# Kernel tuning notes

Hardware: AMD Instinct MI355X
Metric: run time of the kernel (lower is better)

## Reference

```python
import jax, jax.numpy as jnp
import numpy as np

D_MODEL = 2048
N_EXPERTS = 64
TOP_K = 2
AUX_LOSS_COEF = 0.01
ENTROPY_COEF = 0.01


def setup_inputs() -> dict:
    key = jax.random.key(0)
    kx, kw = jax.random.split(key)
    x = jax.random.normal(kx, (4, 4096, D_MODEL), dtype=jnp.float32)
    # nn.Linear(d_model, n_experts, bias=False) weight: [E, D]
    W = jax.random.normal(kw, (N_EXPERTS, D_MODEL), dtype=jnp.float32) * 0.02
    temp = jnp.ones((1,), dtype=jnp.float32)
    return {"x": x, "W": W, "temp": temp}


def reference(x, W, temp):
    B, S, D = x.shape
    E = W.shape[0]
    # gate logits: [B,S,E]
    logits = jnp.einsum("bsd,ed->bse", x, W)
    t = jnp.clip(temp, 0.1, 5.0)  # self.temp.clamp(0.1, 5.0); eval mode -> no noise
    probs = jax.nn.softmax(logits / t, axis=-1)
    expert_probs, expert_indices = jax.lax.top_k(probs, TOP_K)  # [B,S,K]
    # scatter ones at top-k indices -> [B,S,E]
    expert_mask = jax.nn.one_hot(expert_indices, E, dtype=probs.dtype).sum(axis=-2)
    # aux losses
    importance = probs.mean(axis=(0, 1))                 # [E]
    load = expert_mask.sum(axis=(0, 1)) / (B * S + 1e-6)  # [E]
    aux_load_loss = (importance * load).sum() * E * AUX_LOSS_COEF
    token_entropy = -(probs * jnp.log(jnp.clip(probs, 1e-8))).sum(axis=-1).mean()
    router_entropy = token_entropy * ENTROPY_COEF
    return (expert_probs, expert_indices, expert_mask, aux_load_loss, router_entropy)
```

## Files before the change

### kernel.cpp

```cpp
#include <hip/hip_runtime.h>
#include <hip/hip_bf16.h>
#include <math.h>

#define D_MODEL 2048
#define N_EXP   64
#define NTOK    16384
#define NBLK    512
#define NSTG    16

typedef short bf16x8 __attribute__((ext_vector_type(8)));
typedef float f32x16 __attribute__((ext_vector_type(16)));
typedef unsigned int u32;

#define OFF_PROBS 0
#define OFF_IDX   32768
#define OFF_MASK  65536
#define OFF_AUX   1114112
#define OFF_ENT   1114113

#define WF_PS 16384

#define MEMFENCE asm volatile("" ::: "memory")
#define FULLBAR() do { MEMFENCE; __builtin_amdgcn_s_barrier(); MEMFENCE; \
                       __builtin_amdgcn_sched_barrier(0); } while (0)

__device__ __forceinline__ void split3(float xv, u32& h, u32& m, u32& l) {
  u32 xb = __builtin_bit_cast(u32, xv);
  u32 hb = xb & 0xFFFF0000u;
  float tf = xv - __builtin_bit_cast(float, hb);
  u32 tb = __builtin_bit_cast(u32, tf);
  u32 mb = tb & 0xFFFF0000u;
  float t2 = tf - __builtin_bit_cast(float, mb);
  u32 lb = __builtin_bit_cast(u32, t2);
  h = hb >> 16; m = mb >> 16; l = lb >> 16;
}

__device__ __forceinline__ bool better(float a, int ia, float b, int ib) {
  return (a > b) || (a == b && ia < ib);
}

__global__ __launch_bounds__(256) void wprep_kernel(
    const float* __restrict__ W, bf16x8* __restrict__ Wf) {
  int gid  = blockIdx.x * 256 + threadIdx.x;
  int g    = gid >> 7;
  int n    = (gid >> 6) & 1;
  int lane = gid & 63;
  int e    = n * 32 + (lane & 31);
  int k    = g * 16 + ((lane >> 5) << 3);
  const float* wr = W + (size_t)e * D_MODEL + k;
  bf16x8 hv, mv, lv;
#pragma unroll
  for (int j = 0; j < 8; ++j) {
    u32 h, m, l;
    split3(wr[j], h, m, l);
    hv[j] = (short)h; mv[j] = (short)m; lv[j] = (short)l;
  }
  Wf[gid]             = hv;
  Wf[WF_PS + gid]     = mv;
  Wf[2 * WF_PS + gid] = lv;
}

__global__ __launch_bounds__(512, 4) void fused_kernel(
    const float* __restrict__ x, const bf16x8* __restrict__ Wf,
    const float* __restrict__ temp, float* __restrict__ out,
    float* __restrict__ imp_part, float* __restrict__ load_part,
    float* __restrict__ ent_part) {
  __shared__ float lds[16384];
  const int tid  = threadIdx.x;
  const int w    = tid >> 6;
  const int lane = tid & 63;
  const int t0   = blockIdx.x * 32;
  const int rl   = lane & 31;
  const int hg   = lane >> 5;

  float tv = temp[0];
  tv = fminf(fmaxf(tv, 0.1f), 5.0f);
  const float invT = 1.0f / tv;

  const float* gsrc[2];
#pragma unroll
  for (int i = 0; i < 2; ++i) {
    int r0  = w * 4 + i * 2;
    int row = r0 + hg;
    int sc  = rl ^ (row & 31);
    gsrc[i] = x + (size_t)(t0 + row) * D_MODEL + sc * 4;
  }

  auto stage = [&](int st) {
    const int buf = st & 3;
#pragma unroll
    for (int i = 0; i < 2; ++i) {
      int r0 = w * 4 + i * 2;
      __builtin_amdgcn_global_load_lds(
          (const __attribute__((address_space(1))) void*)(gsrc[i] + st * 128),
          (__attribute__((address_space(3))) void*)(lds + buf * 4096 + r0 * 128),
          16, 0, 0);
    }
  };
  auto loadB = [&](int st, bf16x8* bb) {
    const bf16x8* wp = Wf + (size_t)(st * 8 + w) * 128 + lane;
#pragma unroll
    for (int p = 0; p < 3; ++p)
#pragma unroll
      for (int n = 0; n < 2; ++n)
        bb[p * 2 + n] = wp[p * WF_PS + n * 64];
  };

  f32x16 acc0, acc1;
#pragma unroll
  for (int i = 0; i < 16; ++i) { acc0[i] = 0.0f; acc1[i] = 0.0f; }

  bf16x8 b[2][6];
  stage(0); stage(1);
  loadB(0, b[0]);
  asm volatile("s_waitcnt vmcnt(8)" ::: "memory");
  FULLBAR();

  const int c0 = w * 4 + hg * 2;

#pragma unroll
  for (int st = 0; st < NSTG; ++st) {
    if (st + 1 < NSTG) loadB(st + 1, b[(st + 1) & 1]);
    if (st + 2 < NSTG) stage(st + 2);

    const float* rb = lds + (st & 3) * 4096 + rl * 128;
    float4 a0 = *(const float4*)(rb + ((c0 ^ rl) << 2));
    float4 a1 = *(const float4*)(rb + (((c0 + 1) ^ rl) << 2));
    float av[8] = {a0.x, a0.y, a0.z, a0.w, a1.x, a1.y, a1.z, a1.w};
    bf16x8 ah, am, al;
#pragma unroll
    for (int j = 0; j < 8; ++j) {
      u32 hh, mm, ll;
      split3(av[j], hh, mm, ll);
      ah[j] = (short)hh; am[j] = (short)mm; al[j] = (short)ll;
    }
    const bf16x8* bb = b[st & 1];
    acc0 = __builtin_amdgcn_mfma_f32_32x32x16_bf16(ah, bb[0], acc0, 0, 0, 0);
    acc1 = __builtin_amdgcn_mfma_f32_32x32x16_bf16(ah, bb[1], acc1, 0, 0, 0);
    acc0 = __builtin_amdgcn_mfma_f32_32x32x16_bf16(ah, bb[2], acc0, 0, 0, 0);
    acc1 = __builtin_amdgcn_mfma_f32_32x32x16_bf16(ah, bb[3], acc1, 0, 0, 0);
    acc0 = __builtin_amdgcn_mfma_f32_32x32x16_bf16(am, bb[0], acc0, 0, 0, 0);
    acc1 = __builtin_amdgcn_mfma_f32_32x32x16_bf16(am, bb[1], acc1, 0, 0, 0);
    acc0 = __builtin_amdgcn_mfma_f32_32x32x16_bf16(am, bb[2], acc0, 0, 0, 0);
    acc1 = __builtin_amdgcn_mfma_f32_32x32x16_bf16(am, bb[3], acc1, 0, 0, 0);
    acc0 = __builtin_amdgcn_mfma_f32_32x32x16_bf16(ah, bb[4], acc0, 0, 0, 0);
    acc1 = __builtin_amdgcn_mfma_f32_32x32x16_bf16(ah, bb[5], acc1, 0, 0, 0);
    acc0 = __builtin_amdgcn_mfma_f32_32x32x16_bf16(al, bb[0], acc0, 0, 0, 0);
    acc1 = __builtin_amdgcn_mfma_f32_32x32x16_bf16(al, bb[1], acc1, 0, 0, 0);

    if (st < NSTG - 2) {
      asm volatile("s_waitcnt vmcnt(8)" ::: "memory");
      FULLBAR();
    } else if (st == NSTG - 2) {
      asm volatile("s_waitcnt vmcnt(6)" ::: "memory");
      FULLBAR();
    }
  }

  __syncthreads();
#pragma unroll
  for (int r = 0; r < 16; ++r) {
    int row = (r & 3) + ((r >> 2) << 3) + (hg << 2);
    lds[w * 2048 + row * 64 + rl]      = acc0[r];
    lds[w * 2048 + row * 64 + 32 + rl] = acc1[r];
  }
  __syncthreads();

  const int row  = tid >> 4;
  const int colq = tid & 15;
  float l0 = 0.f, l1 = 0.f, l2 = 0.f, l3 = 0.f;
  for (int wv = 0; wv < 8; ++wv) {
    float4 v = *(const float4*)&lds[wv * 2048 + row * 64 + colq * 4];
    l0 += v.x; l1 += v.y; l2 += v.z; l3 += v.w;
  }
  l0 *= invT; l1 *= invT; l2 *= invT; l3 *= invT;

  float m = fmaxf(fmaxf(l0, l1), fmaxf(l2, l3));
#pragma unroll
  for (int d = 1; d < 16; d <<= 1) m = fmaxf(m, __shfl_xor(m, d));

  float ls0 = l0 - m, ls1 = l1 - m, ls2 = l2 - m, ls3 = l3 - m;
  float e0 = __expf(ls0), e1 = __expf(ls1), e2 = __expf(ls2), e3 = __expf(ls3);
  float ssum = e0 + e1 + e2 + e3;
  float dot  = e0 * ls0 + e1 * ls1 + e2 * ls2 + e3 * ls3;
#pragma unroll
  for (int d = 1; d < 16; d <<= 1) {
    ssum += __shfl_xor(ssum, d);
    dot  += __shfl_xor(dot, d);
  }
  const float inv_s = 1.0f / ssum;
  const float ent = __logf(ssum) - dot * inv_s;

  const int eb = colq * 4;
  float b1 = e0, b2 = -1.0f;
  int   i1 = eb, i2 = eb + 1;
  {
    float ev[3] = {e1, e2, e3};
#pragma unroll
    for (int j = 0; j < 3; ++j) {
      int ej = eb + 1 + j;
      if (better(ev[j], ej, b1, i1)) { b2 = b1; i2 = i1; b1 = ev[j]; i1 = ej; }
      else if (better(ev[j], ej, b2, i2)) { b2 = ev[j]; i2 = ej; }
    }
  }
#pragma unroll
  for (int d = 1; d < 16; d <<= 1) {
    float ob1 = __shfl_xor(b1, d), ob2 = __shfl_xor(b2, d);
    int   oi1 = __shfl_xor(i1, d), oi2 = __shfl_xor(i2, d);
    if (better(ob1, oi1, b1, i1)) {
      if (better(b1, i1, ob2, oi2)) { b2 = b1; i2 = i1; }
      else                          { b2 = ob2; i2 = oi2; }
      b1 = ob1; i1 = oi1;
    } else if (better(ob1, oi1, b2, i2)) {
      b2 = ob1; i2 = oi1;
    }
  }

  const int t = t0 + row;
  if (colq == 0) {
    out[OFF_PROBS + (size_t)t * 2 + 0] = b1 * inv_s;
    out[OFF_PROBS + (size_t)t * 2 + 1] = b2 * inv_s;
    out[OFF_IDX   + (size_t)t * 2 + 0] = (float)i1;
    out[OFF_IDX   + (size_t)t * 2 + 1] = (float)i2;
  }
  {
    float4 mv;
    mv.x = ((eb + 0 == i1) || (eb + 0 == i2)) ? 1.0f : 0.0f;
    mv.y = ((eb + 1 == i1) || (eb + 1 == i2)) ? 1.0f : 0.0f;
    mv.z = ((eb + 2 == i1) || (eb + 2 == i2)) ? 1.0f : 0.0f;
    mv.w = ((eb + 3 == i1) || (eb + 3 == i2)) ? 1.0f : 0.0f;
    *(float4*)&out[OFF_MASK + (size_t)t * N_EXP + eb] = mv;
  }

  __syncthreads();
  {
    float4 p4;
    p4.x = e0 * inv_s; p4.y = e1 * inv_s; p4.z = e2 * inv_s; p4.w = e3 * inv_s;
    *(float4*)&lds[row * 64 + eb] = p4;
  }
  if (colq == 0) {
    lds[2048 + row] = (float)i1;
    lds[2080 + row] = (float)i2;
    lds[2112 + row] = ent;
  }
  __syncthreads();
  if (tid < 64) {
    float simp = 0.0f, sld = 0.0f;
    const float fe = (float)tid;
    for (int r = 0; r < 32; ++r) simp += lds[r * 64 + tid];
    for (int r = 0; r < 32; ++r)
      sld += ((lds[2048 + r] == fe) ? 1.0f : 0.0f)
           + ((lds[2080 + r] == fe) ? 1.0f : 0.0f);
    imp_part[blockIdx.x * N_EXP + tid]  = simp;
    load_part[blockIdx.x * N_EXP + tid] = sld;
    float v = (tid < 32) ? lds[2112 + tid] : 0.0f;
#pragma unroll
    for (int d = 1; d < 64; d <<= 1) v += __shfl_xor(v, d);
    if (tid == 0) ent_part[blockIdx.x] = v;
  }
}

__global__ __launch_bounds__(256) void finalize_part(
    const float* __restrict__ imp_part, const float* __restrict__ load_part,
    const float* __restrict__ ent_part, float* __restrict__ imp2,
    float* __restrict__ load2, float* __restrict__ ent2) {
  __shared__ float si[4][64], sl[4][64], se[4];
  const int tid  = threadIdx.x;
  const int lane = tid & 63;
  const int q    = tid >> 6;
  const int base = blockIdx.x * 8 + q * 2;
  float a = imp_part[(size_t)base * N_EXP + lane]
          + imp_part[(size_t)(base + 1) * N_EXP + lane];
  float b = load_part[(size_t)base * N_EXP + lane]
          + load_part[(size_t)(base + 1) * N_EXP + lane];
  si[q][lane] = a;
  sl[q][lane] = b;
  if (lane == 0) se[q] = ent_part[base] + ent_part[base + 1];
  __syncthreads();
  if (tid < 64) {
    imp2[blockIdx.x * N_EXP + tid]  = si[0][tid] + si[1][tid] + si[2][tid] + si[3][tid];
    load2[blockIdx.x * N_EXP + tid] = sl[0][tid] + sl[1][tid] + sl[2][tid] + sl[3][tid];
    if (tid == 0) ent2[blockIdx.x] = se[0] + se[1] + se[2] + se[3];
  }
}

__global__ __launch_bounds__(256) void finalize_final(
    const float* __restrict__ imp2, const float* __restrict__ load2,
    const float* __restrict__ ent2, float* __restrict__ out) {
  __shared__ float si[4][64], sl[4][64];
  const int tid  = threadIdx.x;
  const int lane = tid & 63;
  const int q    = tid >> 6;
  float a = 0.0f, b = 0.0f;
  for (int r = q * 16; r < q * 16 + 16; ++r) {
    a += imp2[r * N_EXP + lane];
    b += load2[r * N_EXP + lane];
  }
  si[q][lane] = a;
  sl[q][lane] = b;
  __syncthreads();
  if (tid < 64) {
    float imp = si[0][tid] + si[1][tid] + si[2][tid] + si[3][tid];
    float ld  = sl[0][tid] + sl[1][tid] + sl[2][tid] + sl[3][tid];
    imp *= (1.0f / 16384.0f);
    ld  *= (1.0f / (16384.0f + 1e-6f));
    float prod = imp * ld;
    float e = ent2[tid];
#pragma unroll
    for (int d = 1; d < 64; d <<= 1) {
      prod += __shfl_xor(prod, d);
      e    += __shfl_xor(e, d);
    }
    if (tid == 0) {
      out[OFF_AUX] = prod * 64.0f * 0.01f;
      out[OFF_ENT] = (e / 16384.0f) * 0.01f;
    }
  }
}

extern "C" void kernel_launch(void* const* d_in, const int* in_sizes, int n_in,
                              void* d_out, int out_size, void* d_ws, size_t ws_size,
                              hipStream_t stream) {
  const float* x    = (const float*)d_in[0];
  const float* W    = (const float*)d_in[1];
  const float* temp = (const float*)d_in[2];
  float* out = (float*)d_out;
  float* ws  = (float*)d_ws;

  bf16x8* Wf    = (bf16x8*)ws;
  float*  imp   = ws + 196608;
  float*  ldp   = imp + NBLK * N_EXP;
  float*  entp  = ldp + NBLK * N_EXP;
  float*  imp2  = entp + NBLK;
  float*  load2 = imp2 + 64 * N_EXP;
  float*  ent2  = load2 + 64 * N_EXP;

  wprep_kernel<<<64, 256, 0, stream>>>(W, Wf);
  fused_kernel<<<NBLK, 512, 0, stream>>>(x, Wf, temp, out, imp, ldp, entp);
  finalize_part<<<64, 256, 0, stream>>>(imp, ldp, entp, imp2, load2, ent2);
  finalize_final<<<1, 256, 0, stream>>>(imp2, load2, ent2, out);
}
```

Before: 50.84 us.

## Give each wave a private x staging region and drop per-stage block barriers

Each wave now stages only the x slice it consumes into its own LDS region, four buffers deep, so the workgroup-wide s_barrier after every stage is removed. Synchronisation becomes per-wave vmcnt waits with prefetch distance 3 instead of 2. This is meant to remove barrier stalls and let waves drift independently. The cost is more outstanding loads per wave and reliance on exact vmcnt counting, since global_load_lds completion is only tracked per wave.

```diff
diff --git a/kernel.cpp b/kernel.cpp
--- a/kernel.cpp
+++ b/kernel.cpp
@@ -19,10 +19,6 @@
 #define OFF_ENT   1114113
 
 #define WF_PS 16384
-
-#define MEMFENCE asm volatile("" ::: "memory")
-#define FULLBAR() do { MEMFENCE; __builtin_amdgcn_s_barrier(); MEMFENCE; \
-                       __builtin_amdgcn_sched_barrier(0); } while (0)
 
 __device__ __forceinline__ void split3(float xv, u32& h, u32& m, u32& l) {
   u32 xb = __builtin_bit_cast(u32, xv);
@@ -80,20 +76,19 @@
   const float* gsrc[2];
 #pragma unroll
   for (int i = 0; i < 2; ++i) {
-    int r0  = w * 4 + i * 2;
-    int row = r0 + hg;
-    int sc  = rl ^ (row & 31);
-    gsrc[i] = x + (size_t)(t0 + row) * D_MODEL + sc * 4;
-  }
-
-  auto stage = [&](int st) {
-    const int buf = st & 3;
+    int tl = i * 16 + (lane >> 2);
+    gsrc[i] = x + (size_t)(t0 + tl) * D_MODEL + w * 16
+            + (((lane & 3) ^ (tl & 3)) << 2);
+  }
+  float* const wbase = lds + w * 2048;
+
+  auto stageW = [&](int s) {
+    float* dst = wbase + (s & 3) * 512;
 #pragma unroll
     for (int i = 0; i < 2; ++i) {
-      int r0 = w * 4 + i * 2;
       __builtin_amdgcn_global_load_lds(
-          (const __attribute__((address_space(1))) void*)(gsrc[i] + st * 128),
-          (__attribute__((address_space(3))) void*)(lds + buf * 4096 + r0 * 128),
+          (const __attribute__((address_space(1))) void*)(gsrc[i] + s * 128),
+          (__attribute__((address_space(3))) void*)(dst + i * 256),
           16, 0, 0);
     }
   };
@@ -111,21 +106,23 @@
   for (int i = 0; i < 16; ++i) { acc0[i] = 0.0f; acc1[i] = 0.0f; }
 
   bf16x8 b[2][6];
-  stage(0); stage(1);
+  stageW(0); stageW(1); stageW(2);
   loadB(0, b[0]);
-  asm volatile("s_waitcnt vmcnt(8)" ::: "memory");
-  FULLBAR();
-
-  const int c0 = w * 4 + hg * 2;
 
 #pragma unroll
   for (int st = 0; st < NSTG; ++st) {
+    if (st + 3 < NSTG) stageW(st + 3);
     if (st + 1 < NSTG) loadB(st + 1, b[(st + 1) & 1]);
-    if (st + 2 < NSTG) stage(st + 2);
-
-    const float* rb = lds + (st & 3) * 4096 + rl * 128;
-    float4 a0 = *(const float4*)(rb + ((c0 ^ rl) << 2));
-    float4 a1 = *(const float4*)(rb + (((c0 + 1) ^ rl) << 2));
+
+    if (st <= 12)      asm volatile("s_waitcnt vmcnt(18)" ::: "memory");
+    else if (st == 13) asm volatile("s_waitcnt vmcnt(16)" ::: "memory");
+    else if (st == 14) asm volatile("s_waitcnt vmcnt(14)" ::: "memory");
+    else               asm volatile("s_waitcnt vmcnt(6)"  ::: "memory");
+    __builtin_amdgcn_sched_barrier(0);
+
+    const float* rb = wbase + (st & 3) * 512 + rl * 16;
+    float4 a0 = *(const float4*)(rb + (((hg * 2)     ^ (rl & 3)) << 2));
+    float4 a1 = *(const float4*)(rb + (((hg * 2 + 1) ^ (rl & 3)) << 2));
     float av[8] = {a0.x, a0.y, a0.z, a0.w, a1.x, a1.y, a1.z, a1.w};
     bf16x8 ah, am, al;
 #pragma unroll
@@ -147,14 +144,6 @@
     acc1 = __builtin_amdgcn_mfma_f32_32x32x16_bf16(ah, bb[5], acc1, 0, 0, 0);
     acc0 = __builtin_amdgcn_mfma_f32_32x32x16_bf16(al, bb[0], acc0, 0, 0, 0);
     acc1 = __builtin_amdgcn_mfma_f32_32x32x16_bf16(al, bb[1], acc1, 0, 0, 0);
-
-    if (st < NSTG - 2) {
-      asm volatile("s_waitcnt vmcnt(8)" ::: "memory");
-      FULLBAR();
-    } else if (st == NSTG - 2) {
-      asm volatile("s_waitcnt vmcnt(6)" ::: "memory");
-      FULLBAR();
-    }
   }
 
   __syncthreads();
```

After: 53.39 us. +5.0%, slower.

## Fuse finalize reductions into main kernel via atomic ticket last-block pattern

Applied to the files above, without the earlier changes.

Removes the two separate finalize kernel launches and does the reductions inside the fused kernel. Each group of 8 blocks takes an atomic ticket, and the last arriving block of a group reduces that group's partials. A second ticket then lets the last group-finisher compute the final aux and entropy scalars. Tickets are zeroed in the weight-prep kernel. This saves two kernel launches and their gaps, at the cost of extra fences and atomics at the end of every block.

```diff
diff --git a/kernel.cpp b/kernel.cpp
--- a/kernel.cpp
+++ b/kernel.cpp
@@ -40,7 +40,9 @@
 }
 
 __global__ __launch_bounds__(256) void wprep_kernel(
-    const float* __restrict__ W, bf16x8* __restrict__ Wf) {
+    const float* __restrict__ W, bf16x8* __restrict__ Wf,
+    u32* __restrict__ tickets) {
+  if (blockIdx.x == 0 && threadIdx.x < 65) tickets[threadIdx.x] = 0u;
   int gid  = blockIdx.x * 256 + threadIdx.x;
   int g    = gid >> 7;
   int n    = (gid >> 6) & 1;
@@ -64,7 +66,9 @@
     const float* __restrict__ x, const bf16x8* __restrict__ Wf,
     const float* __restrict__ temp, float* __restrict__ out,
     float* __restrict__ imp_part, float* __restrict__ load_part,
-    float* __restrict__ ent_part) {
+    float* __restrict__ ent_part, float* __restrict__ imp2,
+    float* __restrict__ load2, float* __restrict__ ent2,
+    u32* __restrict__ tickets) {
   __shared__ float lds[16384];
   const int tid  = threadIdx.x;
   const int w    = tid >> 6;
@@ -258,62 +262,74 @@
     for (int d = 1; d < 64; d <<= 1) v += __shfl_xor(v, d);
     if (tid == 0) ent_part[blockIdx.x] = v;
   }
-}
-
-__global__ __launch_bounds__(256) void finalize_part(
-    const float* __restrict__ imp_part, const float* __restrict__ load_part,
-    const float* __restrict__ ent_part, float* __restrict__ imp2,
-    float* __restrict__ load2, float* __restrict__ ent2) {
-  __shared__ float si[4][64], sl[4][64], se[4];
-  const int tid  = threadIdx.x;
-  const int lane = tid & 63;
-  const int q    = tid >> 6;
-  const int base = blockIdx.x * 8 + q * 2;
-  float a = imp_part[(size_t)base * N_EXP + lane]
-          + imp_part[(size_t)(base + 1) * N_EXP + lane];
-  float b = load_part[(size_t)base * N_EXP + lane]
-          + load_part[(size_t)(base + 1) * N_EXP + lane];
-  si[q][lane] = a;
-  sl[q][lane] = b;
-  if (lane == 0) se[q] = ent_part[base] + ent_part[base + 1];
-  __syncthreads();
-  if (tid < 64) {
-    imp2[blockIdx.x * N_EXP + tid]  = si[0][tid] + si[1][tid] + si[2][tid] + si[3][tid];
-    load2[blockIdx.x * N_EXP + tid] = sl[0][tid] + sl[1][tid] + sl[2][tid] + sl[3][tid];
-    if (tid == 0) ent2[blockIdx.x] = se[0] + se[1] + se[2] + se[3];
-  }
-}
-
-__global__ __launch_bounds__(256) void finalize_final(
-    const float* __restrict__ imp2, const float* __restrict__ load2,
-    const float* __restrict__ ent2, float* __restrict__ out) {
-  __shared__ float si[4][64], sl[4][64];
-  const int tid  = threadIdx.x;
-  const int lane = tid & 63;
-  const int q    = tid >> 6;
-  float a = 0.0f, b = 0.0f;
-  for (int r = q * 16; r < q * 16 + 16; ++r) {
-    a += imp2[r * N_EXP + lane];
-    b += load2[r * N_EXP + lane];
-  }
-  si[q][lane] = a;
-  sl[q][lane] = b;
-  __syncthreads();
-  if (tid < 64) {
-    float imp = si[0][tid] + si[1][tid] + si[2][tid] + si[3][tid];
-    float ld  = sl[0][tid] + sl[1][tid] + sl[2][tid] + sl[3][tid];
-    imp *= (1.0f / 16384.0f);
-    ld  *= (1.0f / (16384.0f + 1e-6f));
-    float prod = imp * ld;
-    float e = ent2[tid];
-#pragma unroll
-    for (int d = 1; d < 64; d <<= 1) {
-      prod += __shfl_xor(prod, d);
-      e    += __shfl_xor(e, d);
-    }
+
+  __syncthreads();
+  const int g = blockIdx.x >> 3;
+  if (tid == 0) {
+    __threadfence();
+    u32 old = atomicAdd(&tickets[g], 1u);
+    lds[0] = (float)old;
+  }
+  __syncthreads();
+  if ((int)lds[0] == 7) {
+    __threadfence();
+    const int b0 = g * 8;
+    if (tid < 64) {
+      float i01 = imp_part[(size_t)(b0+0)*N_EXP+tid] + imp_part[(size_t)(b0+1)*N_EXP+tid];
+      float i23 = imp_part[(size_t)(b0+2)*N_EXP+tid] + imp_part[(size_t)(b0+3)*N_EXP+tid];
+      float i45 = imp_part[(size_t)(b0+4)*N_EXP+tid] + imp_part[(size_t)(b0+5)*N_EXP+tid];
+      float i67 = imp_part[(size_t)(b0+6)*N_EXP+tid] + imp_part[(size_t)(b0+7)*N_EXP+tid];
+      imp2[g * N_EXP + tid] = ((i01 + i23) + i45) + i67;
+      float d01 = load_part[(size_t)(b0+0)*N_EXP+tid] + load_part[(size_t)(b0+1)*N_EXP+tid];
+      float d23 = load_part[(size_t)(b0+2)*N_EXP+tid] + load_part[(size_t)(b0+3)*N_EXP+tid];
+      float d45 = load_part[(size_t)(b0+4)*N_EXP+tid] + load_part[(size_t)(b0+5)*N_EXP+tid];
+      float d67 = load_part[(size_t)(b0+6)*N_EXP+tid] + load_part[(size_t)(b0+7)*N_EXP+tid];
+      load2[g * N_EXP + tid] = ((d01 + d23) + d45) + d67;
+      if (tid == 0) {
+        float e01 = ent_part[b0+0] + ent_part[b0+1];
+        float e23 = ent_part[b0+2] + ent_part[b0+3];
+        float e45 = ent_part[b0+4] + ent_part[b0+5];
+        float e67 = ent_part[b0+6] + ent_part[b0+7];
+        ent2[g] = ((e01 + e23) + e45) + e67;
+      }
+    }
+    __syncthreads();
     if (tid == 0) {
-      out[OFF_AUX] = prod * 64.0f * 0.01f;
-      out[OFF_ENT] = (e / 16384.0f) * 0.01f;
+      __threadfence();
+      u32 fo = atomicAdd(&tickets[64], 1u);
+      lds[0] = (float)fo;
+    }
+    __syncthreads();
+    if ((int)lds[0] == 63) {
+      __threadfence();
+      if (tid < 256) {
+        const int q = tid >> 6, ln = tid & 63;
+        float a = 0.0f, bql = 0.0f;
+        for (int r = q * 16; r < q * 16 + 16; ++r) {
+          a   += imp2[r * N_EXP + ln];
+          bql += load2[r * N_EXP + ln];
+        }
+        lds[q * 64 + ln]       = a;
+        lds[256 + q * 64 + ln] = bql;
+      }
+      __syncthreads();
+      if (tid < 64) {
+        float imp = lds[tid] + lds[64 + tid] + lds[128 + tid] + lds[192 + tid];
+        float ld  = lds[256 + tid] + lds[320 + tid] + lds[384 + tid] + lds[448 + tid];
+        imp *= (1.0f / 16384.0f);
+        ld  *= (1.0f / (16384.0f + 1e-6f));
+        float prod = imp * ld;
+        float e = ent2[tid];
+#pragma unroll
+        for (int d = 1; d < 64; d <<= 1) {
+          prod += __shfl_xor(prod, d);
+          e    += __shfl_xor(e, d);
+        }
+        if (tid == 0) {
+          out[OFF_AUX] = prod * 64.0f * 0.01f;
+          out[OFF_ENT] = (e / 16384.0f) * 0.01f;
+        }
+      }
     }
   }
 }
@@ -334,9 +350,9 @@
   float*  imp2  = entp + NBLK;
   float*  load2 = imp2 + 64 * N_EXP;
   float*  ent2  = load2 + 64 * N_EXP;
-
-  wprep_kernel<<<64, 256, 0, stream>>>(W, Wf);
-  fused_kernel<<<NBLK, 512, 0, stream>>>(x, Wf, temp, out, imp, ldp, entp);
-  finalize_part<<<64, 256, 0, stream>>>(imp, ldp, entp, imp2, load2, ent2);
-  finalize_final<<<1, 256, 0, stream>>>(imp2, load2, ent2, out);
-}
+  u32*    tick  = (u32*)(ent2 + 64);
+
+  wprep_kernel<<<64, 256, 0, stream>>>(W, Wf, tick);
+  fused_kernel<<<NBLK, 512, 0, stream>>>(x, Wf, temp, out, imp, ldp, entp,
+                                         imp2, load2, ent2, tick);
+}
```

Measured after the change: 127.2 us. 2.5x slower.
